# Kernel tuning notes

Measured on AMD Instinct MI355X. Metric: run time of the kernel, lower is better.

The kernel has to match this reference:

```python
import jax, jax.numpy as jnp
import numpy as np

# BigBird-roberta-base config with block_size=64, 12 layers
B = 1; S = 2048; D = 768; F = 3072; V = 50358
L = 12; H = 12; HD = 64; BS = 64; NB = S // BS; R = 3
NEG = -1.0e9
NKB = 5 + R           # global(2) + window(3) + random(3) key blocks per query block
NK = NKB * BS         # gathered keys per query block


def _block_map(nb, r, seed=0):
    """Static per-query-block key-block indices + dedup mask (first occurrence kept)."""
    rng = np.random.default_rng(seed)
    idx = np.zeros((nb, 5 + r), np.int32)
    dedup = np.ones((nb, 5 + r), np.float32)
    for i in range(nb):
        lst = [0, nb - 1, max(i - 1, 0), i, min(i + 1, nb - 1)]
        cand = np.setdiff1d(np.arange(nb), np.array(lst))
        lst += list(rng.choice(cand, r, replace=False))
        seen = set()
        for j, b in enumerate(lst):
            idx[i, j] = int(b)
            if b in seen:
                dedup[i, j] = 0.0
            seen.add(int(b))
    return idx, dedup

BLK_IDX, BLK_DEDUP = _block_map(NB, R)


def layer_norm(x, s, b):
    m = jnp.mean(x, axis=-1, keepdims=True)
    v = jnp.mean(jnp.square(x - m), axis=-1, keepdims=True)
    return (x - m) * jax.lax.rsqrt(v + 1e-12) * s + b


def bigbird_attn(x, wq, wk, wv, bq, bk, bv, wo, bo, key_mask):
    # x: [B,S,D]; key_mask: [B,S] float (1=keep)
    q = (x @ wq + bq).reshape(B, S, H, HD).transpose(0, 2, 1, 3)  # [B,H,S,HD]
    k = (x @ wk + bk).reshape(B, S, H, HD).transpose(0, 2, 1, 3)
    v = (x @ wv + bv).reshape(B, S, H, HD).transpose(0, 2, 1, 3)
    scale = 1.0 / np.sqrt(HD)
    qb = q.reshape(B, H, NB, BS, HD)
    kb = k.reshape(B, H, NB, BS, HD)
    vb = v.reshape(B, H, NB, BS, HD)
    # gather sparse key/value blocks: [B,H,NB,NKB,BS,HD] -> [B,H,NB,NK,HD]
    kg = kb[:, :, BLK_IDX].reshape(B, H, NB, NK, HD)
    vg = vb[:, :, BLK_IDX].reshape(B, H, NB, NK, HD)
    scores = jnp.einsum('bhnqd,bhnkd->bhnqk', qb, kg) * scale  # [B,H,NB,BS,NK]
    kmb = key_mask.reshape(B, NB, BS)[:, BLK_IDX]               # [B,NB,NKB,BS]
    m = (kmb * BLK_DEDUP[None, :, :, None]).reshape(B, 1, NB, 1, NK)
    probs = jax.nn.softmax(scores + (1.0 - m) * NEG, axis=-1)
    ctx = jnp.einsum('bhnqk,bhnkd->bhnqd', probs, vg)           # [B,H,NB,BS,HD]
    # global query blocks (first & last) attend densely to all keys
    qg = jnp.concatenate([qb[:, :, 0], qb[:, :, -1]], axis=2)   # [B,H,2*BS,HD]
    sg = jnp.einsum('bhqd,bhkd->bhqk', qg, k) * scale
    sg = sg + (1.0 - key_mask[:, None, None, :]) * NEG
    cg = jnp.einsum('bhqk,bhkd->bhqd', jax.nn.softmax(sg, axis=-1), v)
    ctx = ctx.at[:, :, 0].set(cg[:, :, :BS]).at[:, :, -1].set(cg[:, :, BS:])
    ctx = ctx.reshape(B, H, S, HD).transpose(0, 2, 1, 3).reshape(B, S, D)
    return ctx @ wo + bo


def setup_inputs() -> dict:
    key = jax.random.key(0)
    ks = jax.random.split(key, 16)
    p = lambda k, shape: jax.random.normal(k, shape, jnp.float32) * 0.02
    return {
        'input_ids': jax.random.randint(ks[0], (B, S), 0, V),
        'attention_mask': jnp.ones((B, S), jnp.int32),
        'token_type_ids': jnp.zeros((B, S), jnp.int32),
        'word_emb': p(ks[1], (V, D)),
        'pos_emb': p(ks[2], (S, D)),
        'type_emb': p(ks[3], (2, D)),
        'emb_ln_s': jnp.ones((D,)), 'emb_ln_b': jnp.zeros((D,)),
        'Wq': p(ks[4], (L, D, D)), 'Wk': p(ks[5], (L, D, D)), 'Wv': p(ks[6], (L, D, D)),
        'bq': jnp.zeros((L, D)), 'bk': jnp.zeros((L, D)), 'bv': jnp.zeros((L, D)),
        'Wo': p(ks[7], (L, D, D)), 'bo': jnp.zeros((L, D)),
        'ln1_s': jnp.ones((L, D)), 'ln1_b': jnp.zeros((L, D)),
        'W1': p(ks[8], (L, D, F)), 'b1': jnp.zeros((L, F)),
        'W2': p(ks[9], (L, F, D)), 'b2': jnp.zeros((L, D)),
        'ln2_s': jnp.ones((L, D)), 'ln2_b': jnp.zeros((L, D)),
        'fc_w': p(ks[10], (D, V)), 'fc_b': jnp.zeros((V,)),
    }


def reference(input_ids, attention_mask, token_type_ids, word_emb, pos_emb, type_emb,
              emb_ln_s, emb_ln_b, Wq, Wk, Wv, bq, bk, bv, Wo, bo, ln1_s, ln1_b,
              W1, b1, W2, b2, ln2_s, ln2_b, fc_w, fc_b):
    x = word_emb[input_ids] + pos_emb[None] + type_emb[token_type_ids]
    x = layer_norm(x, emb_ln_s, emb_ln_b)
    km = attention_mask.astype(x.dtype)
    for l in range(L):
        a = bigbird_attn(x, Wq[l], Wk[l], Wv[l], bq[l], bk[l], bv[l], Wo[l], bo[l], km)
        x = layer_norm(x + a, ln1_s[l], ln1_b[l])
        hdd = jax.nn.gelu(x @ W1[l] + b1[l])
        x = layer_norm(x + hdd @ W2[l] + b2[l], ln2_s[l], ln2_b[l])
    return x @ fc_w + fc_b  # logits [B,S,V]
```

## Files before the change

### kernel.cpp

```cpp
#include <hip/hip_runtime.h>
#include <hip/hip_bf16.h>


#define S_LEN 2048
#define DMODEL 768
#define FFDIM 3072
#define VOCAB 50358
#define VPAD  50432
#define NLAYER 12
#define NHEAD 12
#define NB 32
#define NKB 8
#define QKVN 2304

typedef __attribute__((ext_vector_type(8))) short bfrag8;
typedef __attribute__((ext_vector_type(8))) unsigned short us8;
typedef __attribute__((ext_vector_type(4))) float facc4;

__device__ __forceinline__ unsigned short f2bf(float f) {
  unsigned int u = __builtin_bit_cast(unsigned int, f);
  u += 0x7fffu + ((u >> 16) & 1u);
  return (unsigned short)(u >> 16);
}
__device__ __forceinline__ float bf2f(unsigned short h) {
  unsigned int u = ((unsigned int)h) << 16;
  return __builtin_bit_cast(float, u);
}

#define MFMA16(a, b, c) __builtin_amdgcn_mfma_f32_16x16x32_bf16((a), (b), (c), 0, 0, 0)
#define GLDS16(g, l) __builtin_amdgcn_global_load_lds( \
    (const __attribute__((address_space(1))) void*)(g), \
    (__attribute__((address_space(3))) void*)(l), 16, 0, 0)

struct Pcg {
  unsigned long long hi, lo, inc_hi, inc_lo;
  int has32; unsigned int buf32;
};

__device__ __forceinline__ void pcg_step(Pcg& p) {
  const unsigned long long MH = 0x2360ed051fc65da4ull;
  const unsigned long long ML = 0x4385df649fccf645ull;
  unsigned long long rl = p.lo * ML;
  unsigned long long rh = __umul64hi(p.lo, ML) + p.lo * MH + p.hi * ML;
  unsigned long long nl = rl + p.inc_lo;
  unsigned long long nh = rh + p.inc_hi + (nl < rl ? 1ull : 0ull);
  p.lo = nl; p.hi = nh;
}
__device__ __forceinline__ unsigned long long pcg_next64(Pcg& p) {
  pcg_step(p);
  unsigned int rot = (unsigned int)(p.hi >> 58);
  unsigned long long x = p.hi ^ p.lo;
  return (x >> rot) | (x << ((64u - rot) & 63u));
}
__device__ __forceinline__ unsigned int pcg_next32(Pcg& p) {
  if (p.has32) { p.has32 = 0; return p.buf32; }
  unsigned long long n = pcg_next64(p);
  p.has32 = 1; p.buf32 = (unsigned int)(n >> 32);
  return (unsigned int)n;
}
__device__ __forceinline__ unsigned int lemire32(Pcg& p, unsigned int rng) {
  unsigned int rng_excl = rng + 1u;
  unsigned long long m = (unsigned long long)pcg_next32(p) * (unsigned long long)rng_excl;
  unsigned int leftover = (unsigned int)m;
  if (leftover < rng_excl) {
    unsigned int threshold = (0xffffffffu - rng) % rng_excl;
    while (leftover < threshold) {
      m = (unsigned long long)pcg_next32(p) * (unsigned long long)rng_excl;
      leftover = (unsigned int)m;
    }
  }
  return (unsigned int)(m >> 32);
}

__global__ void blockmap_kernel(int* __restrict__ blk_idx, float* __restrict__ dedup) {
  if (threadIdx.x != 0 || blockIdx.x != 0) return;
  unsigned int pool[4];
  unsigned int hc = 0x43b0d7e5u;
  auto ss_hash = [&hc](unsigned int val) {
    val ^= hc; hc *= 0x931e8875u; val *= hc; val ^= val >> 16; return val;
  };
  auto ss_mix = [](unsigned int x, unsigned int y) {
    unsigned int r = 0xca01f9ddu * x - 0x4973f715u * y;
    r ^= r >> 16; return r;
  };
  for (int i = 0; i < 4; ++i) pool[i] = ss_hash(0u);
  for (int s = 0; s < 4; ++s)
    for (int d = 0; d < 4; ++d)
      if (s != d) pool[d] = ss_mix(pool[d], ss_hash(pool[s]));
  unsigned int st32[8];
  unsigned int hb = 0x8b51f9ddu;
  for (int i = 0; i < 8; ++i) {
    unsigned int dv = pool[i & 3];
    dv ^= hb; hb *= 0x58f38dedu; dv *= hb; dv ^= dv >> 16;
    st32[i] = dv;
  }
  unsigned long long sd[4];
  for (int i = 0; i < 4; ++i)
    sd[i] = (unsigned long long)st32[2*i] | ((unsigned long long)st32[2*i+1] << 32);
  Pcg p;
  p.inc_hi = (sd[2] << 1) | (sd[3] >> 63);
  p.inc_lo = (sd[3] << 1) | 1ull;
  p.hi = 0ull; p.lo = 0ull;
  pcg_step(p);
  unsigned long long ol = p.lo;
  p.lo = ol + sd[1];
  p.hi = p.hi + sd[0] + (p.lo < ol ? 1ull : 0ull);
  pcg_step(p);
  p.has32 = 0; p.buf32 = 0;

  for (int i = 0; i < NB; ++i) {
    int lst[8];
    lst[0] = 0; lst[1] = NB - 1;
    lst[2] = (i > 0) ? i - 1 : 0;
    lst[3] = i;
    lst[4] = (i + 1 < NB - 1) ? i + 1 : NB - 1;
    bool excl[NB];
    for (int c = 0; c < NB; ++c) excl[c] = false;
    for (int j = 0; j < 5; ++j) excl[lst[j]] = true;
    int cand[NB], n = 0;
    for (int c = 0; c < NB; ++c) if (!excl[c]) cand[n++] = c;
    long long idx[3];
    unsigned long long hs[4] = {~0ull, ~0ull, ~0ull, ~0ull};
    for (int tI = 0; tI < 3; ++tI) {
      unsigned long long j = (unsigned long long)(n - 3 + tI);
      unsigned long long val = (unsigned long long)lemire32(p, (unsigned int)j);
      unsigned long long loc = val & 3ull;
      while (hs[loc] != ~0ull && hs[loc] != val) loc = (loc + 1ull) & 3ull;
      if (hs[loc] == ~0ull) { hs[loc] = val; idx[tI] = (long long)val; }
      else {
        loc = j & 3ull;
        while (hs[loc] != ~0ull) loc = (loc + 1ull) & 3ull;
        hs[loc] = j; idx[tI] = (long long)j;
      }
    }
    for (int fi = 2; fi >= 1; --fi) {
      int fj = (int)lemire32(p, (unsigned int)fi);
      long long tmpv = idx[fi]; idx[fi] = idx[fj]; idx[fj] = tmpv;
    }
    lst[5] = cand[idx[0]]; lst[6] = cand[idx[1]]; lst[7] = cand[idx[2]];

    unsigned int seen = 0u;
    for (int j = 0; j < 8; ++j) {
      blk_idx[i*8 + j] = lst[j];
      dedup[i*8 + j] = ((seen >> lst[j]) & 1u) ? 0.0f : 1.0f;
      seen |= (1u << lst[j]);
    }
  }
}

__global__ __launch_bounds__(256) void tconv_kernel(
    const float* __restrict__ src, unsigned short* __restrict__ dst,
    int K, int N, size_t src_stride, size_t dst_stride) {
  __shared__ float tile[64][65];
  src += (size_t)blockIdx.z * src_stride;
  dst += (size_t)blockIdx.z * dst_stride;
  int n0 = blockIdx.x * 64, k0 = blockIdx.y * 64;
  int t = threadIdx.x;
  int tr = t >> 4, tc = (t & 15) * 4;
  if ((N & 3) == 0 && n0 + 64 <= N) {
    #pragma unroll
    for (int i = 0; i < 4; ++i) {
      int k = k0 + tr + i * 16;
      float4 v = *reinterpret_cast<const float4*>(src + (size_t)k * N + n0 + tc);
      tile[tr + i*16][tc + 0] = v.x; tile[tr + i*16][tc + 1] = v.y;
      tile[tr + i*16][tc + 2] = v.z; tile[tr + i*16][tc + 3] = v.w;
    }
  } else if ((N & 1) == 0 && n0 + 64 <= N) {
    #pragma unroll
    for (int i = 0; i < 4; ++i) {
      int k = k0 + tr + i * 16;
      float2 v0 = *reinterpret_cast<const float2*>(src + (size_t)k * N + n0 + tc);
      float2 v1 = *reinterpret_cast<const float2*>(src + (size_t)k * N + n0 + tc + 2);
      tile[tr + i*16][tc + 0] = v0.x; tile[tr + i*16][tc + 1] = v0.y;
      tile[tr + i*16][tc + 2] = v1.x; tile[tr + i*16][tc + 3] = v1.y;
    }
  } else {
    for (int i = 0; i < 4; ++i) {
      int k = k0 + tr + i * 16;
      #pragma unroll
      for (int q2 = 0; q2 < 4; ++q2) {
        int n = n0 + tc + q2;
        tile[tr + i*16][tc + q2] = (n < N) ? src[(size_t)k * N + n] : 0.0f;
      }
    }
  }
  __syncthreads();
  int wr_ = t >> 2, wc_ = (t & 3) * 16;
  us8 w0, w1;
  #pragma unroll
  for (int j = 0; j < 8; ++j) {
    w0[j] = f2bf(tile[wc_ + j][wr_]);
    w1[j] = f2bf(tile[wc_ + 8 + j][wr_]);
  }
  size_t b = (size_t)(n0 + wr_) * K + k0 + wc_;
  *reinterpret_cast<us8*>(dst + b) = w0;
  *reinterpret_cast<us8*>(dst + b + 8) = w1;
}

__global__ void bias_cat_kernel(const float* __restrict__ bq, const float* __restrict__ bk,
                                const float* __restrict__ bv, float* __restrict__ dst) {
  int l = blockIdx.x;
  for (int i = threadIdx.x; i < QKVN; i += blockDim.x) {
    float v = (i < 768) ? bq[l*768 + i] : (i < 1536) ? bk[l*768 + i - 768] : bv[l*768 + i - 1536];
    dst[l*QKVN + i] = v;
  }
}

__device__ __forceinline__ float block_sum256(float v, float* red) {
  for (int off = 32; off > 0; off >>= 1) v += __shfl_down(v, off);
  int wv = threadIdx.x >> 6;
  if ((threadIdx.x & 63) == 0) red[wv] = v;
  __syncthreads();
  float r = red[0] + red[1] + red[2] + red[3];
  __syncthreads();
  return r;
}

__global__ void embed_ln_kernel(const int* __restrict__ ids, const int* __restrict__ tts,
                                const float* __restrict__ we, const float* __restrict__ pe,
                                const float* __restrict__ te, const float* __restrict__ lns,
                                const float* __restrict__ lnb, float* __restrict__ x,
                                unsigned short* __restrict__ xh) {
  __shared__ float red[4];
  int row = blockIdx.x, t = threadIdx.x;
  int id = ids[row], ty = tts[row];
  float e[3]; float s = 0.0f;
  for (int j = 0; j < 3; ++j) {
    int d = t + 256*j;
    e[j] = we[(size_t)id*DMODEL + d] + pe[(size_t)row*DMODEL + d] + te[(size_t)ty*DMODEL + d];
    s += e[j];
  }
  float mean = block_sum256(s, red) * (1.0f/768.0f);
  float vs = 0.0f;
  for (int j = 0; j < 3; ++j) { float dd = e[j] - mean; vs += dd*dd; }
  float var = block_sum256(vs, red) * (1.0f/768.0f);
  float inv = rsqrtf(var + 1e-12f);
  for (int j = 0; j < 3; ++j) {
    int d = t + 256*j;
    float val = (e[j] - mean) * inv * lns[d] + lnb[d];
    size_t idx = (size_t)row*DMODEL + d;
    x[idx] = val;
    xh[idx] = f2bf(val);
  }
}

__global__ void resln_kernel(float* __restrict__ x, const float* __restrict__ a,
                             const float* __restrict__ lns, const float* __restrict__ lnb,
                             unsigned short* __restrict__ xh) {
  __shared__ float red[4];
  int row = blockIdx.x, t = threadIdx.x;
  float e[3]; float s = 0.0f;
  for (int j = 0; j < 3; ++j) {
    int d = t + 256*j;
    e[j] = x[(size_t)row*DMODEL + d] + a[(size_t)row*DMODEL + d];
    s += e[j];
  }
  float mean = block_sum256(s, red) * (1.0f/768.0f);
  float vs = 0.0f;
  for (int j = 0; j < 3; ++j) { float dd = e[j] - mean; vs += dd*dd; }
  float var = block_sum256(vs, red) * (1.0f/768.0f);
  float inv = rsqrtf(var + 1e-12f);
  for (int j = 0; j < 3; ++j) {
    int d = t + 256*j;
    float val = (e[j] - mean) * inv * lns[d] + lnb[d];
    size_t idx = (size_t)row*DMODEL + d;
    x[idx] = val;
    xh[idx] = f2bf(val);
  }
}

template<int BM, int NBUF, int TN, int OMODE, int ACT>
__global__ __launch_bounds__(256) void gemm13_kernel(
    const unsigned short* __restrict__ A_g, const unsigned short* __restrict__ Bt,
    const float* __restrict__ bias,
    float* __restrict__ Cf, unsigned short* __restrict__ Ch,
    int K, int Nreal) {
  __shared__ alignas(16) unsigned short As[NBUF][BM][32];
  __shared__ alignas(16) unsigned short Bs[NBUF][TN][32];
  constexpr int MFR = BM / 32;
  constexpr int NFR = (TN == 128) ? 4 : 2;
  constexpr int ACALLS = BM / 64;
  constexpr int NLOADS = ACALLS + ((TN == 128) ? 2 : 1);
  constexpr int DEPTH = NBUF - 2;
  int t = threadIdx.x;
  int mb = (int)gridDim.x;
  int nwg = mb * (int)gridDim.y;
  int lin = (int)blockIdx.x + mb * (int)blockIdx.y;
  int cpx = nwg >> 3;
  int nl = (lin & 7) * cpx + (lin >> 3);
  int m0 = (nl % mb) * BM, n0 = (nl / mb) * TN;

  int wave = t >> 6, lane = t & 63, l16 = lane & 15, lk = lane >> 4;
  int wr = wave >> 1, wc = wave & 1;
  int row16 = lane >> 2, seg4 = lane & 3;
  const int srcoff = (seg4 ^ ((row16 >> 1) & 3)) * 8;
  const int swzrd = (lk ^ ((l16 >> 1) & 3)) * 8;

  const unsigned short* ag = A_g + (size_t)(m0 + wave*(BM/4) + row16) * K + srcoff;
  const unsigned short* bg = Bt + (size_t)(n0 + (TN == 128 ? wave*32 : wave*16) + row16) * K + srcoff;
  const size_t K16 = (size_t)16 * K;

  auto STAGE = [&](int buf, int kit) {
    int k0 = kit << 5;
    #pragma unroll
    for (int j = 0; j < ACALLS; ++j)
      GLDS16(ag + (size_t)j * K16 + k0, &As[buf][wave*(BM/4) + 16*j][0]);
    if constexpr (TN == 128) {
      GLDS16(bg + k0, &Bs[buf][wave*32][0]);
      GLDS16(bg + K16 + k0, &Bs[buf][wave*32 + 16][0]);
    } else {
      GLDS16(bg + k0, &Bs[buf][wave*16][0]);
    }
  };

  facc4 acc[MFR][NFR];
  #pragma unroll
  for (int mi = 0; mi < MFR; ++mi)
    #pragma unroll
    for (int ni = 0; ni < NFR; ++ni)
      acc[mi][ni] = (facc4){0.f, 0.f, 0.f, 0.f};

  const int nk = K >> 5;
  STAGE(0, 0);
  if constexpr (DEPTH == 2) STAGE(1, 1);
  int cur = 0;
  for (int it = 0; it < nk; ++it) {
    if constexpr (DEPTH == 2) {
      if (it + 2 < nk) {
        STAGE((cur + 2) % NBUF, it + 2);
        asm volatile("s_waitcnt vmcnt(%0)" :: "n"(2 * NLOADS) : "memory");
      } else if (it + 1 < nk) {
        asm volatile("s_waitcnt vmcnt(%0)" :: "n"(NLOADS) : "memory");
      } else {
        asm volatile("s_waitcnt vmcnt(0)" ::: "memory");
      }
    } else {
      if (it + 1 < nk) {
        STAGE((cur + 1) % NBUF, it + 1);
        asm volatile("s_waitcnt vmcnt(%0)" :: "n"(NLOADS) : "memory");
      } else {
        asm volatile("s_waitcnt vmcnt(0)" ::: "memory");
      }
    }
    __builtin_amdgcn_sched_barrier(0);
    __builtin_amdgcn_s_barrier();
    __builtin_amdgcn_sched_barrier(0);
    bfrag8 af[MFR], bf[NFR];
    #pragma unroll
    for (int mi = 0; mi < MFR; ++mi)
      af[mi] = *reinterpret_cast<const bfrag8*>(&As[cur][wr*(BM/2) + mi*16 + l16][swzrd]);
    #pragma unroll
    for (int ni = 0; ni < NFR; ++ni)
      bf[ni] = *reinterpret_cast<const bfrag8*>(&Bs[cur][(TN == 128 ? wc*64 : wc*32) + ni*16 + l16][swzrd]);
    #pragma unroll
    for (int mi = 0; mi < MFR; ++mi)
      #pragma unroll
      for (int ni = 0; ni < NFR; ++ni)
        acc[mi][ni] = MFMA16(af[mi], bf[ni], acc[mi][ni]);
    cur = (cur + 1) % NBUF;
  }

  #pragma unroll
  for (int mi = 0; mi < MFR; ++mi)
    #pragma unroll
    for (int ni = 0; ni < NFR; ++ni) {
      int col = n0 + (TN == 128 ? wc*64 : wc*32) + ni*16 + l16;
      if (col >= Nreal) continue;
      float bv = bias[col];
      #pragma unroll
      for (int r2 = 0; r2 < 4; ++r2) {
        int row = m0 + wr*(BM/2) + mi*16 + lk*4 + r2;
        float val = acc[mi][ni][r2] + bv;
        if (ACT == 1) {
          float xx = val;
          val = 0.5f * xx * (1.0f + tanhf(0.7978845608028654f * (xx + 0.044715f * xx * xx * xx)));
        }
        size_t idx = (size_t)row * Nreal + col;
        if (OMODE == 0) Cf[idx] = val;
        else Ch[idx] = f2bf(val);
      }
    }
}

__device__ __forceinline__ void stage_glds64_swz(unsigned short (*dst)[64],
    const unsigned short* __restrict__ src, int ld, int t) {
  int w = t >> 6, lane = t & 63;
  int row8 = lane >> 3;
  int seg = (lane & 7) ^ (row8 & 7);
  const unsigned short* s = src + (size_t)(w*16 + row8) * ld + seg * 8;
  GLDS16(s, &dst[w*16][0]);
  GLDS16(s + (size_t)8 * ld, &dst[w*16 + 8][0]);
}

__global__ __launch_bounds__(256) void attn_kernel(
    const unsigned short* __restrict__ qkvh,
    const int* __restrict__ blk_idx, const float* __restrict__ dedup,
    const int* __restrict__ amask,
    unsigned short* __restrict__ ctxh,
    float* __restrict__ go, float* __restrict__ gm, float* __restrict__ gl) {
  __shared__ alignas(16) unsigned short Qs[64][64];
  __shared__ alignas(16) unsigned short KVs[64][64];
  __shared__ alignas(16) unsigned short Vs[64][66];
  __shared__ alignas(16) unsigned short Pt[64][68];
  int h = blockIdx.y;
  int bx = (int)blockIdx.x;
  const bool is_glob = (bx >= 30);
  int g = is_glob ? ((bx - 30) >> 2) : 0;
  int part = is_glob ? ((bx - 30) & 3) : 0;
  int qi = is_glob ? (g ? (NB - 1) : 0) : (bx + 1);
  int t = threadIdx.x, wave = t >> 6, lane = t & 63, l16 = lane & 15, lk = lane >> 4;
  const int swq0 = ((lk ^ (l16 & 7))) * 8;
  const int swq1 = (((4 + lk) ^ (l16 & 7))) * 8;
  const int vrow = t >> 2, vcolb = (t & 3) * 16;

  stage_glds64_swz(Qs, qkvh + (size_t)(qi*64)*QKVN + h*64, QKVN, t);
  __syncthreads();
  const bfrag8 q0 = *reinterpret_cast<const bfrag8*>(&Qs[wave*16 + l16][swq0]);
  const bfrag8 q1 = *reinterpret_cast<const bfrag8*>(&Qs[wave*16 + l16][swq1]);

  float mrow[4] = {-3.0e38f, -3.0e38f, -3.0e38f, -3.0e38f};
  float lrow[4] = {0.f, 0.f, 0.f, 0.f};
  facc4 o[4];
  #pragma unroll
  for (int ni = 0; ni < 4; ++ni) o[ni] = (facc4){0.f, 0.f, 0.f, 0.f};

  for (int kb = 0; kb < 8; ++kb) {
    int b; float dd;
    if (is_glob) { b = part*8 + kb; dd = 1.0f; }
    else { b = blk_idx[qi*NKB + kb]; dd = dedup[qi*NKB + kb]; }
    __builtin_amdgcn_s_barrier();
    stage_glds64_swz(KVs, qkvh + (size_t)(b*64)*QKVN + DMODEL + h*64, QKVN, t);
    __builtin_amdgcn_sched_barrier(0);
    const unsigned short* vsrc = qkvh + (size_t)(b*64 + vrow)*QKVN + 2*DMODEL + h*64 + vcolb;
    us8 v0 = *reinterpret_cast<const us8*>(vsrc);
    us8 v1 = *reinterpret_cast<const us8*>(vsrc + 8);
    asm volatile("s_waitcnt vmcnt(2)" ::: "memory");
    __builtin_amdgcn_sched_barrier(0);
    __builtin_amdgcn_s_barrier();
    float s[4][4];
    #pragma unroll
    for (int ni = 0; ni < 4; ++ni) {
      bfrag8 k0 = *reinterpret_cast<const bfrag8*>(&KVs[ni*16 + l16][swq0]);
      bfrag8 k1 = *reinterpret_cast<const bfrag8*>(&KVs[ni*16 + l16][swq1]);
      facc4 sa = (facc4){0.f, 0.f, 0.f, 0.f};
      sa = MFMA16(q0, k0, sa);
      sa = MFMA16(q1, k1, sa);
      int colk = ni*16 + l16;
      float mk = (float)amask[b*64 + colk] * dd;
      float addm = (1.0f - mk) * (-1.0e9f);
      #pragma unroll
      for (int r = 0; r < 4; ++r) s[ni][r] = sa[r] * 0.125f + addm;
    }
    float pexp[4][4];
    #pragma unroll
    for (int r = 0; r < 4; ++r) {
      float tm = fmaxf(fmaxf(s[0][r], s[1][r]), fmaxf(s[2][r], s[3][r]));
      tm = fmaxf(tm, __shfl_xor(tm, 1));
      tm = fmaxf(tm, __shfl_xor(tm, 2));
      tm = fmaxf(tm, __shfl_xor(tm, 4));
      tm = fmaxf(tm, __shfl_xor(tm, 8));
      float mn = fmaxf(mrow[r], tm);
      float f = expf(mrow[r] - mn);
      #pragma unroll
      for (int ni = 0; ni < 4; ++ni) o[ni][r] *= f;
      float ps = 0.0f;
      #pragma unroll
      for (int ni = 0; ni < 4; ++ni) { pexp[ni][r] = expf(s[ni][r] - mn); ps += pexp[ni][r]; }
      ps += __shfl_xor(ps, 1);
      ps += __shfl_xor(ps, 2);
      ps += __shfl_xor(ps, 4);
      ps += __shfl_xor(ps, 8);
      lrow[r] = lrow[r] * f + ps;
      mrow[r] = mn;
    }
    #pragma unroll
    for (int ni = 0; ni < 4; ++ni)
      #pragma unroll
      for (int r = 0; r < 4; ++r)
        Pt[wave*16 + lk*4 + r][ni*16 + l16] = f2bf(pexp[ni][r]);
    #pragma unroll
    for (int j = 0; j < 8; ++j) {
      Vs[vcolb + j][vrow] = v0[j];
      Vs[vcolb + 8 + j][vrow] = v1[j];
    }
    asm volatile("s_waitcnt lgkmcnt(0)" ::: "memory");
    __builtin_amdgcn_sched_barrier(0);
    __builtin_amdgcn_s_barrier();
    #pragma unroll
    for (int kc = 0; kc < 2; ++kc) {
      bfrag8 ph = *reinterpret_cast<const bfrag8*>(&Pt[wave*16 + l16][kc*32 + lk*8]);
      #pragma unroll
      for (int ni = 0; ni < 4; ++ni) {
        bfrag8 vh = *reinterpret_cast<const bfrag8*>(&Vs[ni*16 + l16][kc*32 + lk*8]);
        o[ni] = MFMA16(ph, vh, o[ni]);
      }
    }
  }

  if (!is_glob) {
    float invl[4];
    #pragma unroll
    for (int r = 0; r < 4; ++r) invl[r] = 1.0f / lrow[r];
    #pragma unroll
    for (int ni = 0; ni < 4; ++ni)
      #pragma unroll
      for (int r = 0; r < 4; ++r) {
        int row = qi*64 + wave*16 + lk*4 + r;
        int col = h*64 + ni*16 + l16;
        ctxh[(size_t)row*DMODEL + col] = f2bf(o[ni][r] * invl[r]);
      }
  } else {
    int pidx = (g * NHEAD + h) * 4 + part;
    float* gob = go + (size_t)pidx * 64 * 64;
    #pragma unroll
    for (int ni = 0; ni < 4; ++ni)
      #pragma unroll
      for (int r = 0; r < 4; ++r)
        gob[(wave*16 + lk*4 + r) * 64 + ni*16 + l16] = o[ni][r];
    if (l16 == 0) {
      #pragma unroll
      for (int r = 0; r < 4; ++r) {
        int row = wave*16 + lk*4 + r;
        gm[pidx*64 + row] = mrow[r];
        gl[pidx*64 + row] = lrow[r];
      }
    }
  }
}

__global__ __launch_bounds__(256) void gattn_comb_kernel(
    const float* __restrict__ go, const float* __restrict__ gm,
    const float* __restrict__ gl, unsigned short* __restrict__ ctxh) {
  int g = blockIdx.x, h = blockIdx.y;
  int t = threadIdx.x;
  int row = t >> 2, cseg = (t & 3) * 16;
  int base = (g * NHEAD + h) * 4;
  float m = -3.0e38f;
  for (int p = 0; p < 4; ++p) m = fmaxf(m, gm[(base + p)*64 + row]);
  float w[4]; float l = 0.0f;
  for (int p = 0; p < 4; ++p) {
    w[p] = expf(gm[(base + p)*64 + row] - m);
    l += gl[(base + p)*64 + row] * w[p];
  }
  float inv = 1.0f / l;
  int qrow = (g ? (NB - 1) * 64 : 0) + row;
  for (int c = 0; c < 16; ++c) {
    float acc = 0.0f;
    for (int p = 0; p < 4; ++p)
      acc += go[((size_t)(base + p)*64 + row)*64 + cseg + c] * w[p];
    ctxh[(size_t)qrow*DMODEL + h*64 + cseg + c] = f2bf(acc * inv);
  }
}

extern "C" void kernel_launch(void* const* d_in, const int* in_sizes, int n_in,
                              void* d_out, int out_size, void* d_ws, size_t ws_size,
                              hipStream_t stream) {
  const int*   input_ids  = (const int*)d_in[0];
  const int*   attn_mask  = (const int*)d_in[1];
  const int*   token_type = (const int*)d_in[2];
  const float* word_emb   = (const float*)d_in[3];
  const float* pos_emb    = (const float*)d_in[4];
  const float* type_emb   = (const float*)d_in[5];
  const float* emb_ln_s   = (const float*)d_in[6];
  const float* emb_ln_b   = (const float*)d_in[7];
  const float* Wq = (const float*)d_in[8];
  const float* Wk = (const float*)d_in[9];
  const float* Wv = (const float*)d_in[10];
  const float* bq = (const float*)d_in[11];
  const float* bk = (const float*)d_in[12];
  const float* bv = (const float*)d_in[13];
  const float* Wo = (const float*)d_in[14];
  const float* bo = (const float*)d_in[15];
  const float* ln1_s = (const float*)d_in[16];
  const float* ln1_b = (const float*)d_in[17];
  const float* W1 = (const float*)d_in[18];
  const float* b1 = (const float*)d_in[19];
  const float* W2 = (const float*)d_in[20];
  const float* b2 = (const float*)d_in[21];
  const float* ln2_s = (const float*)d_in[22];
  const float* ln2_b = (const float*)d_in[23];
  const float* fc_w = (const float*)d_in[24];
  const float* fc_b = (const float*)d_in[25];
  float* out = (float*)d_out;

  unsigned char* base = (unsigned char*)d_ws;
  size_t off = 0;
  auto carve = [&](size_t bytes) -> void* {
    void* p = base + off;
    off = (off + bytes + 255) & ~(size_t)255;
    return p;
  };
  int*   blk_i = (int*)carve(256 * 4);
  float* dedup = (float*)carve(256 * 4);
  float* bqkv  = (float*)carve((size_t)NLAYER * QKVN * 4);
  float* x     = (float*)carve((size_t)S_LEN * DMODEL * 4);
  float* tmp   = (float*)carve((size_t)S_LEN * DMODEL * 4);
  unsigned short* xh   = (unsigned short*)carve((size_t)S_LEN * DMODEL * 2);
  unsigned short* qkvh = (unsigned short*)carve((size_t)S_LEN * QKVN * 2);
  unsigned short* ctxh = (unsigned short*)carve((size_t)S_LEN * DMODEL * 2);
  unsigned short* hbh  = (unsigned short*)carve((size_t)S_LEN * FFDIM * 2);
  float* go    = (float*)carve((size_t)2 * NHEAD * 4 * 64 * 64 * 4);
  float* gm    = (float*)carve((size_t)2 * NHEAD * 4 * 64 * 4);
  float* gl    = (float*)carve((size_t)2 * NHEAD * 4 * 64 * 4);
  unsigned short* qkvT = (unsigned short*)carve((size_t)NLAYER * QKVN * DMODEL * 2);
  unsigned short* woT  = (unsigned short*)carve((size_t)NLAYER * DMODEL * DMODEL * 2);
  unsigned short* w1T  = (unsigned short*)carve((size_t)NLAYER * FFDIM * DMODEL * 2);
  unsigned short* w2T  = (unsigned short*)carve((size_t)NLAYER * DMODEL * FFDIM * 2);
  unsigned short* fcT  = (unsigned short*)carve((size_t)VPAD * DMODEL * 2);

  blockmap_kernel<<<1, 1, 0, stream>>>(blk_i, dedup);

  const size_t DD = (size_t)DMODEL * DMODEL;
  dim3 g768(12, 12, NLAYER);
  tconv_kernel<<<g768, 256, 0, stream>>>(Wq, qkvT + 0,            DMODEL, DMODEL, DD, (size_t)QKVN * DMODEL);
  tconv_kernel<<<g768, 256, 0, stream>>>(Wk, qkvT + 768 * DMODEL, DMODEL, DMODEL, DD, (size_t)QKVN * DMODEL);
  tconv_kernel<<<g768, 256, 0, stream>>>(Wv, qkvT + 1536 * DMODEL,DMODEL, DMODEL, DD, (size_t)QKVN * DMODEL);
  tconv_kernel<<<g768, 256, 0, stream>>>(Wo, woT, DMODEL, DMODEL, DD, DD);
  tconv_kernel<<<dim3(48, 12, NLAYER), 256, 0, stream>>>(W1, w1T, DMODEL, FFDIM, (size_t)DMODEL * FFDIM, (size_t)FFDIM * DMODEL);
  tconv_kernel<<<dim3(12, 48, NLAYER), 256, 0, stream>>>(W2, w2T, FFDIM, DMODEL, (size_t)FFDIM * DMODEL, (size_t)DMODEL * FFDIM);
  tconv_kernel<<<dim3(VPAD / 64, 12, 1), 256, 0, stream>>>(fc_w, fcT, DMODEL, VOCAB, 0, 0);
  bias_cat_kernel<<<NLAYER, 256, 0, stream>>>(bq, bk, bv, bqkv);

  embed_ln_kernel<<<S_LEN, 256, 0, stream>>>(input_ids, token_type, word_emb, pos_emb,
                                             type_emb, emb_ln_s, emb_ln_b, x, xh);

  for (int l = 0; l < NLAYER; ++l) {
    gemm13_kernel<64, 4, 128, 2, 0><<<dim3(32, QKVN/128), 256, 0, stream>>>(
        xh, qkvT + (size_t)l * QKVN * DMODEL, bqkv + (size_t)l * QKVN,
        nullptr, qkvh, DMODEL, QKVN);

    attn_kernel<<<dim3(38, NHEAD), 256, 0, stream>>>(
        qkvh, blk_i, dedup, attn_mask, ctxh, go, gm, gl);
    gattn_comb_kernel<<<dim3(2, NHEAD), 256, 0, stream>>>(go, gm, gl, ctxh);

    gemm13_kernel<64, 4, 64, 0, 0><<<dim3(32, DMODEL/64), 256, 0, stream>>>(
        ctxh, woT + (size_t)l * DD, bo + (size_t)l * DMODEL,
        tmp, nullptr, DMODEL, DMODEL);
    resln_kernel<<<S_LEN, 256, 0, stream>>>(x, tmp, ln1_s + l*DMODEL, ln1_b + l*DMODEL, xh);

    gemm13_kernel<64, 4, 128, 2, 1><<<dim3(32, FFDIM/128), 256, 0, stream>>>(
        xh, w1T + (size_t)l * FFDIM * DMODEL, b1 + (size_t)l * FFDIM,
        nullptr, hbh, DMODEL, FFDIM);
    gemm13_kernel<64, 4, 64, 0, 0><<<dim3(32, DMODEL/64), 256, 0, stream>>>(
        hbh, w2T + (size_t)l * DMODEL * FFDIM, b2 + (size_t)l * DMODEL,
        tmp, nullptr, FFDIM, DMODEL);
    resln_kernel<<<S_LEN, 256, 0, stream>>>(x, tmp, ln2_s + l*DMODEL, ln2_b + l*DMODEL, xh);
  }

  gemm13_kernel<128, 3, 128, 0, 0><<<dim3(16, VPAD/128), 256, 0, stream>>>(
      xh, fcT, fc_b, out, nullptr, DMODEL, VOCAB);
}
```

Before: 2.417 ms.

## Double-buffer K/V block loads in sparse attention kernel and precompute key masks

The attention kernel now prefetches the next key block into a second shared-memory buffer and the next V block into registers while the current block is computed. The loop is fully unrolled with register ping-pong. Block indices and additive mask values for all eight key blocks are computed once up front instead of inside the loop. This hides global-load latency behind the MFMA and softmax work, at the cost of more LDS and more registers, which may lower occupancy. Attention is only one part of the whole-model runtime.

```diff
diff --git a/kernel.cpp b/kernel.cpp
--- a/kernel.cpp
+++ b/kernel.cpp
@@ -399,7 +399,7 @@
     unsigned short* __restrict__ ctxh,
     float* __restrict__ go, float* __restrict__ gm, float* __restrict__ gl) {
   __shared__ alignas(16) unsigned short Qs[64][64];
-  __shared__ alignas(16) unsigned short KVs[64][64];
+  __shared__ alignas(16) unsigned short KV2[2][64][64];
   __shared__ alignas(16) unsigned short Vs[64][66];
   __shared__ alignas(16) unsigned short Pt[64][68];
   int h = blockIdx.y;
@@ -413,6 +413,21 @@
   const int swq1 = (((4 + lk) ^ (l16 & 7))) * 8;
   const int vrow = t >> 2, vcolb = (t & 3) * 16;
 
+  int barr[8];
+  float addm[8][4];
+  #pragma unroll
+  for (int kb = 0; kb < 8; ++kb)
+    barr[kb] = is_glob ? (part*8 + kb) : blk_idx[qi*NKB + kb];
+  #pragma unroll
+  for (int kb = 0; kb < 8; ++kb) {
+    float dd = is_glob ? 1.0f : dedup[qi*NKB + kb];
+    #pragma unroll
+    for (int ni = 0; ni < 4; ++ni) {
+      float mk = (float)amask[barr[kb]*64 + ni*16 + l16] * dd;
+      addm[kb][ni] = (1.0f - mk) * (-1.0e9f);
+    }
+  }
+
   stage_glds64_swz(Qs, qkvh + (size_t)(qi*64)*QKVN + h*64, QKVN, t);
   __syncthreads();
   const bfrag8 q0 = *reinterpret_cast<const bfrag8*>(&Qs[wave*16 + l16][swq0]);
@@ -424,32 +439,40 @@
   #pragma unroll
   for (int ni = 0; ni < 4; ++ni) o[ni] = (facc4){0.f, 0.f, 0.f, 0.f};
 
-  for (int kb = 0; kb < 8; ++kb) {
-    int b; float dd;
-    if (is_glob) { b = part*8 + kb; dd = 1.0f; }
-    else { b = blk_idx[qi*NKB + kb]; dd = dedup[qi*NKB + kb]; }
-    __builtin_amdgcn_s_barrier();
-    stage_glds64_swz(KVs, qkvh + (size_t)(b*64)*QKVN + DMODEL + h*64, QKVN, t);
-    __builtin_amdgcn_sched_barrier(0);
-    const unsigned short* vsrc = qkvh + (size_t)(b*64 + vrow)*QKVN + 2*DMODEL + h*64 + vcolb;
-    us8 v0 = *reinterpret_cast<const us8*>(vsrc);
-    us8 v1 = *reinterpret_cast<const us8*>(vsrc + 8);
-    asm volatile("s_waitcnt vmcnt(2)" ::: "memory");
+  stage_glds64_swz(KV2[0], qkvh + (size_t)(barr[0]*64)*QKVN + DMODEL + h*64, QKVN, t);
+  __builtin_amdgcn_sched_barrier(0);
+  us8 vA0, vA1, vB0, vB1;
+  {
+    const unsigned short* vs0 = qkvh + (size_t)(barr[0]*64 + vrow)*QKVN + 2*DMODEL + h*64 + vcolb;
+    vA0 = *reinterpret_cast<const us8*>(vs0);
+    vA1 = *reinterpret_cast<const us8*>(vs0 + 8);
+  }
+
+  auto body = [&](int kb, const us8& vc0, const us8& vc1, us8& vn0, us8& vn1) {
+    if (kb + 1 < 8) {
+      int bn = barr[kb + 1];
+      stage_glds64_swz(KV2[(kb + 1) & 1], qkvh + (size_t)(bn*64)*QKVN + DMODEL + h*64, QKVN, t);
+      __builtin_amdgcn_sched_barrier(0);
+      const unsigned short* vsn = qkvh + (size_t)(bn*64 + vrow)*QKVN + 2*DMODEL + h*64 + vcolb;
+      vn0 = *reinterpret_cast<const us8*>(vsn);
+      vn1 = *reinterpret_cast<const us8*>(vsn + 8);
+      asm volatile("s_waitcnt vmcnt(4)" ::: "memory");
+    } else {
+      asm volatile("s_waitcnt vmcnt(0)" ::: "memory");
+    }
     __builtin_amdgcn_sched_barrier(0);
     __builtin_amdgcn_s_barrier();
+    __builtin_amdgcn_sched_barrier(0);
     float s[4][4];
     #pragma unroll
     for (int ni = 0; ni < 4; ++ni) {
-      bfrag8 k0 = *reinterpret_cast<const bfrag8*>(&KVs[ni*16 + l16][swq0]);
-      bfrag8 k1 = *reinterpret_cast<const bfrag8*>(&KVs[ni*16 + l16][swq1]);
+      bfrag8 k0 = *reinterpret_cast<const bfrag8*>(&KV2[kb & 1][ni*16 + l16][swq0]);
+      bfrag8 k1 = *reinterpret_cast<const bfrag8*>(&KV2[kb & 1][ni*16 + l16][swq1]);
       facc4 sa = (facc4){0.f, 0.f, 0.f, 0.f};
       sa = MFMA16(q0, k0, sa);
       sa = MFMA16(q1, k1, sa);
-      int colk = ni*16 + l16;
-      float mk = (float)amask[b*64 + colk] * dd;
-      float addm = (1.0f - mk) * (-1.0e9f);
-      #pragma unroll
-      for (int r = 0; r < 4; ++r) s[ni][r] = sa[r] * 0.125f + addm;
+      #pragma unroll
+      for (int r = 0; r < 4; ++r) s[ni][r] = sa[r] * 0.125f + addm[kb][ni];
     }
     float pexp[4][4];
     #pragma unroll
@@ -480,12 +503,13 @@
         Pt[wave*16 + lk*4 + r][ni*16 + l16] = f2bf(pexp[ni][r]);
     #pragma unroll
     for (int j = 0; j < 8; ++j) {
-      Vs[vcolb + j][vrow] = v0[j];
-      Vs[vcolb + 8 + j][vrow] = v1[j];
+      Vs[vcolb + j][vrow] = vc0[j];
+      Vs[vcolb + 8 + j][vrow] = vc1[j];
     }
     asm volatile("s_waitcnt lgkmcnt(0)" ::: "memory");
     __builtin_amdgcn_sched_barrier(0);
     __builtin_amdgcn_s_barrier();
+    __builtin_amdgcn_sched_barrier(0);
     #pragma unroll
     for (int kc = 0; kc < 2; ++kc) {
       bfrag8 ph = *reinterpret_cast<const bfrag8*>(&Pt[wave*16 + l16][kc*32 + lk*8]);
@@ -495,7 +519,16 @@
         o[ni] = MFMA16(ph, vh, o[ni]);
       }
     }
-  }
+  };
+
+  body(0, vA0, vA1, vB0, vB1);
+  body(1, vB0, vB1, vA0, vA1);
+  body(2, vA0, vA1, vB0, vB1);
+  body(3, vB0, vB1, vA0, vA1);
+  body(4, vA0, vA1, vB0, vB1);
+  body(5, vB0, vB1, vA0, vA1);
+  body(6, vA0, vA1, vB0, vB1);
+  body(7, vB0, vB1, vA0, vA1);
 
   if (!is_glob) {
     float invl[4];
```

Result: faster. 2.367 ms (-2.0%).
